# Performance work log

Hardware: AMD Instinct MI355X
Metric: run time of the kernel (lower is better)

## Reference

```python
import jax, jax.numpy as jnp
import numpy as np

LN_EPS = 1e-5
L2_EPS = 1e-6
TAU = 0.07

def _proj(x, W, b, g, be):
    # Linear + LayerNorm (dropout is identity in eval)
    y = x @ W.T + b
    mu = jnp.mean(y, axis=-1, keepdims=True)
    var = jnp.var(y, axis=-1, keepdims=True)
    return (y - mu) * jax.lax.rsqrt(var + LN_EPS) * g + be

def _l2norm(x):
    return x / (jnp.linalg.norm(x, axis=-1, keepdims=True) + L2_EPS)

def setup_inputs() -> dict:
    key = jax.random.key(0)
    ks = iter(jax.random.split(key, 16))
    B, C, D = 2048, 512, 256
    dims = {"text": 1024, "image": 1024, "audio": 512, "tab": 256}
    inp = {}
    for n, d in dims.items():
        inp[f"f_{n}"] = jax.random.normal(next(ks), (B, d), jnp.float32)
        inp[f"W_{n}"] = jax.random.normal(next(ks), (D, d), jnp.float32) * (1.0 / np.sqrt(d))
        inp[f"b_{n}"] = jnp.zeros((D,), jnp.float32)
        inp[f"g_{n}"] = jnp.ones((D,), jnp.float32)
        inp[f"be_{n}"] = jnp.zeros((D,), jnp.float32)
    inp["U"] = jax.random.normal(next(ks), (C, D), jnp.float32) * (1.0 / np.sqrt(D))
    inp["O"] = jax.random.normal(next(ks), (C, D), jnp.float32) * (1.0 / np.sqrt(D))
    inp["cls_bias"] = jnp.zeros((C,), jnp.float32)
    return inp

def reference(f_text, f_image, f_audio, f_tab,
              W_text, b_text, g_text, be_text,
              W_image, b_image, g_image, be_image,
              W_audio, b_audio, g_audio, be_audio,
              W_tab, b_tab, g_tab, be_tab,
              U, O, cls_bias):
    # Per-modality projection -> Z: [B, M, D]
    Z = jnp.stack([
        _proj(f_text, W_text, b_text, g_text, be_text),
        _proj(f_image, W_image, b_image, g_image, be_image),
        _proj(f_audio, W_audio, b_audio, g_audio, be_audio),
        _proj(f_tab, W_tab, b_tab, g_tab, be_tab),
    ], axis=1)
    Zn = _l2norm(Z)            # [B, M, D]
    Un = _l2norm(U)            # [C, D]
    sim = jnp.einsum('bmd,cd->bmc', Zn, Un) / max(TAU, 1e-6)
    r = jax.nn.softmax(sim, axis=1)                 # softmax over modalities M
    Cmix = jnp.einsum('bmc,bmd->bcd', r, Z)         # [B, C, D]
    logits = jnp.einsum('cd,bcd->bc', O, Cmix) + cls_bias
    OjZi = jnp.einsum('cd,bmd->bmc', O, Z)
    contrib = OjZi * r
    return logits, r, sim, contrib
```

## Files before the change

kernel.cpp:

```cpp
#include <hip/hip_runtime.h>
#include <math.h>

typedef __attribute__((ext_vector_type(8))) short short8;
typedef __attribute__((ext_vector_type(4))) float f32x4;
typedef unsigned short u16;

constexpr int Bn = 2048, Mn = 4, Cn = 512, Dn = 256;
constexpr size_t LOGITS_OFF = 0;
constexpr size_t R_OFF   = (size_t)Bn * Cn;
constexpr size_t SIM_OFF = R_OFF + (size_t)Bn * Mn * Cn;
constexpr size_t CTR_OFF = SIM_OFF + (size_t)Bn * Mn * Cn;
constexpr float INV_TAU = 1.0f / 0.07f;

__device__ __forceinline__ unsigned short f2bf(float f) {
  unsigned u = __float_as_uint(f);
  u += 0x7fffu + ((u >> 16) & 1u);
  return (unsigned short)(u >> 16);
}

__device__ __forceinline__ void gload16(const void* g, void* l) {
  __builtin_amdgcn_global_load_lds(
      (const __attribute__((address_space(1))) void*)g,
      (__attribute__((address_space(3))) void*)l, 16, 0, 0);
}

struct CvtArgs {
  const float* src[6];
  u16* dst[6];
};

__global__ __launch_bounds__(256) void cvt_kernel(CvtArgs a,
                                                  const float* __restrict__ U,
                                                  float* __restrict__ invU) {
  const int blk = blockIdx.x;
  if (blk >= 480) {
    int c = (blk - 480) * 4 + (threadIdx.x >> 6);
    int lane = threadIdx.x & 63;
    float4 v = *(const float4*)&U[(size_t)c * Dn + lane * 4];
    float s = v.x*v.x + v.y*v.y + v.z*v.z + v.w*v.w;
    #pragma unroll
    for (int m = 32; m >= 1; m >>= 1) s += __shfl_xor(s, m, 64);
    if (lane == 0) invU[c] = 1.0f / (sqrtf(s) + 1e-6f);
    return;
  }
  int c = blk * 256 + threadIdx.x;
  const int ends[6] = {32768, 65536, 81920, 90112, 106496, 122880};
  int ai = 0, base = 0;
  #pragma unroll
  for (int i = 0; i < 5; i++)
    if (c >= ends[i]) { ai = i + 1; base = ends[i]; }
  int idx = (c - base) * 8;
  const float4* s = (const float4*)(a.src[ai] + idx);
  float4 v0 = s[0], v1 = s[1];
  uint4 p;
  p.x = f2bf(v0.x) | ((unsigned)f2bf(v0.y) << 16);
  p.y = f2bf(v0.z) | ((unsigned)f2bf(v0.w) << 16);
  p.z = f2bf(v1.x) | ((unsigned)f2bf(v1.y) << 16);
  p.w = f2bf(v1.z) | ((unsigned)f2bf(v1.w) << 16);
  *(uint4*)(a.dst[ai] + idx) = p;
}

struct ProjArgs {
  const float* f[4];
  const float* b[4];
  const float* g[4];
  const float* be[4];
  const u16* Wb[4];
  int K[4];
};

__global__ __launch_bounds__(512, 4) void proj_kernel(ProjArgs a,
                                                      u16* __restrict__ Zb,
                                                      float* __restrict__ invZ) {
  const int m = blockIdx.y;
  const int K = a.K[m];
  const int NS = K >> 5;
  const float* __restrict__ F = a.f[m];
  const u16* __restrict__ Wm = a.Wb[m];

  const int tid = threadIdx.x;
  const int w = tid >> 6, l = tid & 63;
  const int rg = l >> 4, c16 = l & 15;
  const int row0 = blockIdx.x * 16;

  __shared__ u16 aS[16 * 1024];
  __shared__ float pS[8][16][2];
  __shared__ float qS[8][16];
  __shared__ u16 zS[16][264];

  const int niter = (K * 16) >> 12;
  for (int it = 0; it < niter; it++) {
    int i = it * 512 + tid;
    int row = i & 15, kc = i >> 4;
    const float* src = F + (size_t)(row0 + row) * K + kc * 8;
    float4 v0 = *(const float4*)src;
    float4 v1 = *(const float4*)(src + 4);
    short8 p;
    p[0] = (short)f2bf(v0.x); p[1] = (short)f2bf(v0.y);
    p[2] = (short)f2bf(v0.z); p[3] = (short)f2bf(v0.w);
    p[4] = (short)f2bf(v1.x); p[5] = (short)f2bf(v1.y);
    p[6] = (short)f2bf(v1.z); p[7] = (short)f2bf(v1.w);
    *(short8*)&aS[i * 8] = p;
  }
  __syncthreads();

  f32x4 acc[2];
  acc[0] = (f32x4){0.f, 0.f, 0.f, 0.f};
  acc[1] = (f32x4){0.f, 0.f, 0.f, 0.f};
  const u16* b0p = Wm + (size_t)(w * 32 + c16) * K + rg * 8;
  const u16* b1p = b0p + (size_t)16 * K;
  const int abase = (rg * 16 + c16) * 8;

  #pragma unroll 4
  for (int t = 0; t < NS; t++) {
    short8 av = *(const short8*)&aS[abase + t * 512];
    short8 b0 = *(const short8*)(b0p + t * 32);
    short8 b1 = *(const short8*)(b1p + t * 32);
    acc[0] = __builtin_amdgcn_mfma_f32_16x16x32_bf16(av, b0, acc[0], 0, 0, 0);
    acc[1] = __builtin_amdgcn_mfma_f32_16x16x32_bf16(av, b1, acc[1], 0, 0, 0);
  }

  float bb[2], gg[2], ee[2];
  #pragma unroll
  for (int nf = 0; nf < 2; nf++) {
    int col = w * 32 + nf * 16 + c16;
    bb[nf] = a.b[m][col];
    gg[nf] = a.g[m][col];
    ee[nf] = a.be[m][col];
  }
  float s[4] = {0,0,0,0}, s2[4] = {0,0,0,0};
  #pragma unroll
  for (int nf = 0; nf < 2; nf++)
    #pragma unroll
    for (int j = 0; j < 4; j++) {
      float y = acc[nf][j] + bb[nf];
      acc[nf][j] = y;
      s[j] += y; s2[j] += y * y;
    }
  #pragma unroll
  for (int msk = 8; msk >= 1; msk >>= 1)
    #pragma unroll
    for (int j = 0; j < 4; j++) {
      s[j]  += __shfl_xor(s[j],  msk, 64);
      s2[j] += __shfl_xor(s2[j], msk, 64);
    }
  if (c16 == 0)
    #pragma unroll
    for (int j = 0; j < 4; j++) {
      pS[w][rg*4+j][0] = s[j];
      pS[w][rg*4+j][1] = s2[j];
    }
  __syncthreads();
  float mu[4], rs[4];
  #pragma unroll
  for (int j = 0; j < 4; j++) {
    int row = rg*4 + j;
    float st = 0.f, s2t = 0.f;
    #pragma unroll
    for (int ww = 0; ww < 8; ww++) { st += pS[ww][row][0]; s2t += pS[ww][row][1]; }
    mu[j] = st * (1.0f/256.0f);
    float var = s2t * (1.0f/256.0f) - mu[j]*mu[j];
    rs[j] = rsqrtf(var + 1e-5f);
  }
  float zs[4] = {0,0,0,0};
  #pragma unroll
  for (int nf = 0; nf < 2; nf++)
    #pragma unroll
    for (int j = 0; j < 4; j++) {
      float z = (acc[nf][j] - mu[j]) * rs[j] * gg[nf] + ee[nf];
      acc[nf][j] = z;
      zs[j] += z * z;
    }
  #pragma unroll
  for (int msk = 8; msk >= 1; msk >>= 1)
    #pragma unroll
    for (int j = 0; j < 4; j++) zs[j] += __shfl_xor(zs[j], msk, 64);
  if (c16 == 0)
    #pragma unroll
    for (int j = 0; j < 4; j++) qS[w][rg*4+j] = zs[j];
  __syncthreads();
  #pragma unroll
  for (int j = 0; j < 4; j++) {
    int row = rg*4 + j;
    float zt = 0.f;
    #pragma unroll
    for (int ww = 0; ww < 8; ww++) zt += qS[ww][row];
    float inv = 1.0f / (sqrtf(zt) + 1e-6f);
    if (c16 == 0 && w == 0)
      invZ[(size_t)(row0 + row) * 4 + m] = inv;
  }
  #pragma unroll
  for (int nf = 0; nf < 2; nf++)
    #pragma unroll
    for (int j = 0; j < 4; j++)
      zS[rg*4 + j][w*32 + nf*16 + c16] = f2bf(acc[nf][j]);
  __syncthreads();
  {
    int row = tid >> 5, colc = (tid & 31) * 8;
    uint4 v = *(const uint4*)&zS[row][colc];
    *(uint4*)(Zb + ((size_t)(row0 + row) * 4 + m) * 256 + colc) = v;
  }
}

__global__ __launch_bounds__(256, 4) void dual_kernel(
    const u16* __restrict__ Zb,
    const u16* __restrict__ Ub,
    const u16* __restrict__ Ob,
    const float* __restrict__ invZ, const float* __restrict__ invU,
    const float* __restrict__ cls_bias, float* __restrict__ out) {
  const int tid = threadIdx.x;
  const int w = tid >> 6, l = tid & 63;
  const int wr = w & 1, wc = w >> 1;
  const int rg = l >> 4, c16 = l & 15;
  const int row0 = blockIdx.x * 64;
  const int col0 = blockIdx.y * 64 + wc * 32;

  __shared__ u16 aS[64 * 256];

  #pragma unroll
  for (int it = 0; it < 8; it++) {
    int i = it * 256 + tid;
    gload16(Zb + (size_t)(row0 + (i & 63)) * 256 + (i >> 6) * 8, &aS[i * 8]);
  }
  __syncthreads();

  f32x4 accU[2][2], accO[2][2];
  #pragma unroll
  for (int i = 0; i < 2; i++)
    #pragma unroll
    for (int j = 0; j < 2; j++) {
      accU[i][j] = (f32x4){0.f, 0.f, 0.f, 0.f};
      accO[i][j] = (f32x4){0.f, 0.f, 0.f, 0.f};
    }
  const u16* u0p = Ub + (size_t)(col0 + c16) * 256 + rg * 8;
  const u16* u1p = u0p + 16 * 256;
  const u16* o0p = Ob + (size_t)(col0 + c16) * 256 + rg * 8;
  const u16* o1p = o0p + 16 * 256;
  const int ab0 = (rg * 64 + wr * 32 + c16) * 8;
  const int ab1 = ab0 + 16 * 8;

  #pragma unroll 4
  for (int t = 0; t < 8; t++) {
    short8 a0 = *(const short8*)&aS[ab0 + t * 2048];
    short8 a1 = *(const short8*)&aS[ab1 + t * 2048];
    short8 u0 = *(const short8*)(u0p + t * 32);
    short8 u1 = *(const short8*)(u1p + t * 32);
    short8 o0 = *(const short8*)(o0p + t * 32);
    short8 o1 = *(const short8*)(o1p + t * 32);
    accU[0][0] = __builtin_amdgcn_mfma_f32_16x16x32_bf16(a0, u0, accU[0][0], 0, 0, 0);
    accU[0][1] = __builtin_amdgcn_mfma_f32_16x16x32_bf16(a0, u1, accU[0][1], 0, 0, 0);
    accU[1][0] = __builtin_amdgcn_mfma_f32_16x16x32_bf16(a1, u0, accU[1][0], 0, 0, 0);
    accU[1][1] = __builtin_amdgcn_mfma_f32_16x16x32_bf16(a1, u1, accU[1][1], 0, 0, 0);
    accO[0][0] = __builtin_amdgcn_mfma_f32_16x16x32_bf16(a0, o0, accO[0][0], 0, 0, 0);
    accO[0][1] = __builtin_amdgcn_mfma_f32_16x16x32_bf16(a0, o1, accO[0][1], 0, 0, 0);
    accO[1][0] = __builtin_amdgcn_mfma_f32_16x16x32_bf16(a1, o0, accO[1][0], 0, 0, 0);
    accO[1][1] = __builtin_amdgcn_mfma_f32_16x16x32_bf16(a1, o1, accO[1][1], 0, 0, 0);
  }

  #pragma unroll
  for (int mf = 0; mf < 2; mf++) {
    const int bmb = row0 + wr * 32 + mf * 16 + rg * 4;
    const f32x4 iz = *(const f32x4*)&invZ[bmb];
    const int bidx = bmb >> 2;
    #pragma unroll
    for (int nf = 0; nf < 2; nf++) {
      int col = col0 + nf * 16 + c16;
      float iu = invU[col] * INV_TAU;
      f32x4 sU = accU[mf][nf], sO = accO[mf][nf];
      float sim0 = sU[0] * iz[0] * iu;
      float sim1 = sU[1] * iz[1] * iu;
      float sim2 = sU[2] * iz[2] * iu;
      float sim3 = sU[3] * iz[3] * iu;
      float mx = fmaxf(fmaxf(sim0, sim1), fmaxf(sim2, sim3));
      float e0 = __expf(sim0 - mx), e1 = __expf(sim1 - mx);
      float e2 = __expf(sim2 - mx), e3 = __expf(sim3 - mx);
      float rinv = 1.0f / (e0 + e1 + e2 + e3);
      float r0 = e0 * rinv, r1 = e1 * rinv, r2 = e2 * rinv, r3 = e3 * rinv;
      float ct0 = sO[0] * r0, ct1 = sO[1] * r1, ct2 = sO[2] * r2, ct3 = sO[3] * r3;
      size_t sb = (size_t)bmb * Cn + col;
      out[SIM_OFF + sb]        = sim0;
      out[SIM_OFF + sb + Cn]   = sim1;
      out[SIM_OFF + sb + 2*Cn] = sim2;
      out[SIM_OFF + sb + 3*Cn] = sim3;
      out[R_OFF + sb]          = r0;
      out[R_OFF + sb + Cn]     = r1;
      out[R_OFF + sb + 2*Cn]   = r2;
      out[R_OFF + sb + 3*Cn]   = r3;
      out[CTR_OFF + sb]        = ct0;
      out[CTR_OFF + sb + Cn]   = ct1;
      out[CTR_OFF + sb + 2*Cn] = ct2;
      out[CTR_OFF + sb + 3*Cn] = ct3;
      out[LOGITS_OFF + (size_t)bidx * Cn + col] =
          ct0 + ct1 + ct2 + ct3 + cls_bias[col];
    }
  }
}

extern "C" void kernel_launch(void* const* d_in, const int* in_sizes, int n_in,
                              void* d_out, int out_size, void* d_ws, size_t ws_size,
                              hipStream_t stream) {
  const int fi[4] = {0, 5, 10, 15};
  const int Ks[4] = {1024, 1024, 512, 256};

  char* ws = (char*)d_ws;
  u16* Zb  = (u16*)(ws + 0);
  u16* Wb0 = (u16*)(ws + 4194304);
  u16* Wb1 = (u16*)(ws + 4718592);
  u16* Wb2 = (u16*)(ws + 5242880);
  u16* Wb3 = (u16*)(ws + 5505024);
  u16* Ub  = (u16*)(ws + 5636096);
  u16* Ob  = (u16*)(ws + 5898240);
  float* invZ = (float*)(ws + 6160384);
  float* invU = (float*)(ws + 6193152);
  u16* Wb[4] = {Wb0, Wb1, Wb2, Wb3};

  ProjArgs pa;
  for (int m = 0; m < 4; m++) {
    pa.f[m]  = (const float*)d_in[fi[m] + 0];
    pa.b[m]  = (const float*)d_in[fi[m] + 2];
    pa.g[m]  = (const float*)d_in[fi[m] + 3];
    pa.be[m] = (const float*)d_in[fi[m] + 4];
    pa.Wb[m] = Wb[m];
    pa.K[m]  = Ks[m];
  }
  const float* U        = (const float*)d_in[20];
  const float* O        = (const float*)d_in[21];
  const float* cls_bias = (const float*)d_in[22];

  CvtArgs ca;
  ca.src[0] = (const float*)d_in[1];   ca.dst[0] = Wb0;
  ca.src[1] = (const float*)d_in[6];   ca.dst[1] = Wb1;
  ca.src[2] = (const float*)d_in[11];  ca.dst[2] = Wb2;
  ca.src[3] = (const float*)d_in[16];  ca.dst[3] = Wb3;
  ca.src[4] = U;                       ca.dst[4] = Ub;
  ca.src[5] = O;                       ca.dst[5] = Ob;

  float* out = (float*)d_out;

  cvt_kernel<<<608, 256, 0, stream>>>(ca, U, invU);
  proj_kernel<<<dim3(Bn / 16, 4), 512, 0, stream>>>(pa, Zb, invZ);
  dual_kernel<<<dim3((Bn * Mn) / 64, Cn / 64), 256, 0, stream>>>(
      Zb, Ub, Ob, invZ, invU, cls_bias, out);
}
```

Before: 171.4 us.

## Pre-swizzle weights and Z into MFMA fragment order, retile proj and dual kernels

The convert kernel now writes the bf16 weights, U and O in MFMA-fragment order, so each lane's B operand is one contiguous 16-byte load. The projection kernel handles 32 rows per block with a 2x2 MFMA tile, which halves weight re-reads, and writes Z in a fragment-swizzled layout. The dual kernel stages U/O tiles in LDS and streams Z fragments straight from global memory, with one 16-row group per wave and a 32-column tile. The cost is larger LDS use in proj, which may lower occupancy, and more complex index math.

```diff
diff --git a/kernel.cpp b/kernel.cpp
--- a/kernel.cpp
+++ b/kernel.cpp
@@ -12,6 +12,8 @@
 constexpr size_t CTR_OFF = SIM_OFF + (size_t)Bn * Mn * Cn;
 constexpr float INV_TAU = 1.0f / 0.07f;
 
+#define MFMA16(av, bv, cv) __builtin_amdgcn_mfma_f32_16x16x32_bf16(av, bv, cv, 0, 0, 0)
+
 __device__ __forceinline__ unsigned short f2bf(float f) {
   unsigned u = __float_as_uint(f);
   u += 0x7fffu + ((u >> 16) & 1u);
@@ -23,6 +25,7 @@
       (const __attribute__((address_space(1))) void*)g,
       (__attribute__((address_space(3))) void*)l, 16, 0, 0);
 }
+
 
 struct CvtArgs {
   const float* src[6];
@@ -45,19 +48,28 @@
   }
   int c = blk * 256 + threadIdx.x;
   const int ends[6] = {32768, 65536, 81920, 90112, 106496, 122880};
+  const int Kv[6]   = {1024, 1024, 512, 256, 256, 256};
+  const int lgNT[6] = {5, 5, 4, 3, 3, 3};
   int ai = 0, base = 0;
   #pragma unroll
   for (int i = 0; i < 5; i++)
     if (c >= ends[i]) { ai = i + 1; base = ends[i]; }
-  int idx = (c - base) * 8;
-  const float4* s = (const float4*)(a.src[ai] + idx);
-  float4 v0 = s[0], v1 = s[1];
+  const int K = Kv[ai], lg = lgNT[ai];
+  int j = c - base;
+  int l = j & 63;
+  int tcg = j >> 6;
+  int t = tcg & ((1 << lg) - 1);
+  int cg = tcg >> lg;
+  int col = cg * 16 + (l & 15);
+  int k0 = t * 32 + (l >> 4) * 8;
+  const float* s = a.src[ai] + (size_t)col * K + k0;
+  float4 v0 = *(const float4*)s, v1 = *(const float4*)(s + 4);
   uint4 p;
   p.x = f2bf(v0.x) | ((unsigned)f2bf(v0.y) << 16);
   p.y = f2bf(v0.z) | ((unsigned)f2bf(v0.w) << 16);
   p.z = f2bf(v1.x) | ((unsigned)f2bf(v1.y) << 16);
   p.w = f2bf(v1.z) | ((unsigned)f2bf(v1.w) << 16);
-  *(uint4*)(a.dst[ai] + idx) = p;
+  *(uint4*)(a.dst[ai] + (size_t)j * 8) = p;
 }
 
 struct ProjArgs {
@@ -65,59 +77,61 @@
   const float* b[4];
   const float* g[4];
   const float* be[4];
-  const u16* Wb[4];
+  const u16* Wt[4];
   int K[4];
 };
 
 __global__ __launch_bounds__(512, 4) void proj_kernel(ProjArgs a,
-                                                      u16* __restrict__ Zb,
+                                                      u16* __restrict__ Zb2,
                                                       float* __restrict__ invZ) {
   const int m = blockIdx.y;
   const int K = a.K[m];
-  const int NS = K >> 5;
+  const int NT = K >> 5;
   const float* __restrict__ F = a.f[m];
-  const u16* __restrict__ Wm = a.Wb[m];
+  const u16* __restrict__ Wt = a.Wt[m];
 
   const int tid = threadIdx.x;
   const int w = tid >> 6, l = tid & 63;
   const int rg = l >> 4, c16 = l & 15;
-  const int row0 = blockIdx.x * 16;
-
-  __shared__ u16 aS[16 * 1024];
-  __shared__ float pS[8][16][2];
-  __shared__ float qS[8][16];
-  __shared__ u16 zS[16][264];
-
-  const int niter = (K * 16) >> 12;
-  for (int it = 0; it < niter; it++) {
-    int i = it * 512 + tid;
-    int row = i & 15, kc = i >> 4;
+  const int row0 = blockIdx.x * 32;
+
+  __shared__ __align__(16) u16 aS[32768];
+  __shared__ float pS[8][32][2];
+  __shared__ float qS[8][32];
+
+  const int nch = K * 4;
+  for (int i = tid; i < nch; i += 512) {
+    int row = i & 31, kc = i >> 5;
     const float* src = F + (size_t)(row0 + row) * K + kc * 8;
-    float4 v0 = *(const float4*)src;
-    float4 v1 = *(const float4*)(src + 4);
+    float4 v0 = *(const float4*)src, v1 = *(const float4*)(src + 4);
     short8 p;
     p[0] = (short)f2bf(v0.x); p[1] = (short)f2bf(v0.y);
     p[2] = (short)f2bf(v0.z); p[3] = (short)f2bf(v0.w);
     p[4] = (short)f2bf(v1.x); p[5] = (short)f2bf(v1.y);
     p[6] = (short)f2bf(v1.z); p[7] = (short)f2bf(v1.w);
-    *(short8*)&aS[i * 8] = p;
-  }
-  __syncthreads();
-
-  f32x4 acc[2];
-  acc[0] = (f32x4){0.f, 0.f, 0.f, 0.f};
-  acc[1] = (f32x4){0.f, 0.f, 0.f, 0.f};
-  const u16* b0p = Wm + (size_t)(w * 32 + c16) * K + rg * 8;
-  const u16* b1p = b0p + (size_t)16 * K;
-  const int abase = (rg * 16 + c16) * 8;
+    *(short8*)&aS[(size_t)i * 8] = p;
+  }
+  __syncthreads();
+
+  f32x4 acc[2][2];
+  #pragma unroll
+  for (int i = 0; i < 2; i++)
+    #pragma unroll
+    for (int j = 0; j < 2; j++) acc[i][j] = (f32x4){0.f, 0.f, 0.f, 0.f};
+
+  const size_t bbase = ((size_t)(w * 2) * NT) * 512 + l * 8;
+  const int a0b = rg * 256 + c16 * 8;
 
   #pragma unroll 4
-  for (int t = 0; t < NS; t++) {
-    short8 av = *(const short8*)&aS[abase + t * 512];
-    short8 b0 = *(const short8*)(b0p + t * 32);
-    short8 b1 = *(const short8*)(b1p + t * 32);
-    acc[0] = __builtin_amdgcn_mfma_f32_16x16x32_bf16(av, b0, acc[0], 0, 0, 0);
-    acc[1] = __builtin_amdgcn_mfma_f32_16x16x32_bf16(av, b1, acc[1], 0, 0, 0);
+  for (int t = 0; t < NT; t++) {
+    short8 a0 = *(const short8*)&aS[a0b + t * 1024];
+    short8 a1 = *(const short8*)&aS[a0b + t * 1024 + 128];
+    short8 b0 = *(const short8*)(Wt + bbase + (size_t)t * 512);
+    short8 b1 = *(const short8*)(Wt + bbase + (size_t)(NT + t) * 512);
+    acc[0][0] = MFMA16(a0, b0, acc[0][0]);
+    acc[0][1] = MFMA16(a0, b1, acc[0][1]);
+    acc[1][0] = MFMA16(a1, b0, acc[1][0]);
+    acc[1][1] = MFMA16(a1, b1, acc[1][1]);
   }
 
   float bb[2], gg[2], ee[2];
@@ -128,171 +142,180 @@
     gg[nf] = a.g[m][col];
     ee[nf] = a.be[m][col];
   }
-  float s[4] = {0,0,0,0}, s2[4] = {0,0,0,0};
-  #pragma unroll
-  for (int nf = 0; nf < 2; nf++)
+  float s[2][4] = {{0,0,0,0},{0,0,0,0}}, s2[2][4] = {{0,0,0,0},{0,0,0,0}};
+  #pragma unroll
+  for (int mf = 0; mf < 2; mf++)
+    #pragma unroll
+    for (int nf = 0; nf < 2; nf++)
+      #pragma unroll
+      for (int j = 0; j < 4; j++) {
+        float y = acc[mf][nf][j] + bb[nf];
+        acc[mf][nf][j] = y;
+        s[mf][j] += y; s2[mf][j] += y * y;
+      }
+  #pragma unroll
+  for (int msk = 8; msk >= 1; msk >>= 1)
+    #pragma unroll
+    for (int mf = 0; mf < 2; mf++)
+      #pragma unroll
+      for (int j = 0; j < 4; j++) {
+        s[mf][j]  += __shfl_xor(s[mf][j],  msk, 64);
+        s2[mf][j] += __shfl_xor(s2[mf][j], msk, 64);
+      }
+  if (c16 == 0)
+    #pragma unroll
+    for (int mf = 0; mf < 2; mf++)
+      #pragma unroll
+      for (int j = 0; j < 4; j++) {
+        int row = mf * 16 + rg * 4 + j;
+        pS[w][row][0] = s[mf][j];
+        pS[w][row][1] = s2[mf][j];
+      }
+  __syncthreads();
+  float mu[2][4], rs[2][4];
+  #pragma unroll
+  for (int mf = 0; mf < 2; mf++)
     #pragma unroll
     for (int j = 0; j < 4; j++) {
-      float y = acc[nf][j] + bb[nf];
-      acc[nf][j] = y;
-      s[j] += y; s2[j] += y * y;
+      int row = mf * 16 + rg * 4 + j;
+      float st = 0.f, s2t = 0.f;
+      #pragma unroll
+      for (int ww = 0; ww < 8; ww++) { st += pS[ww][row][0]; s2t += pS[ww][row][1]; }
+      mu[mf][j] = st * (1.0f / 256.0f);
+      float var = s2t * (1.0f / 256.0f) - mu[mf][j] * mu[mf][j];
+      rs[mf][j] = rsqrtf(var + 1e-5f);
     }
+  float zs[2][4] = {{0,0,0,0},{0,0,0,0}};
+  #pragma unroll
+  for (int mf = 0; mf < 2; mf++)
+    #pragma unroll
+    for (int nf = 0; nf < 2; nf++)
+      #pragma unroll
+      for (int j = 0; j < 4; j++) {
+        float z = (acc[mf][nf][j] - mu[mf][j]) * rs[mf][j] * gg[nf] + ee[nf];
+        acc[mf][nf][j] = z;
+        zs[mf][j] += z * z;
+      }
   #pragma unroll
   for (int msk = 8; msk >= 1; msk >>= 1)
     #pragma unroll
-    for (int j = 0; j < 4; j++) {
-      s[j]  += __shfl_xor(s[j],  msk, 64);
-      s2[j] += __shfl_xor(s2[j], msk, 64);
-    }
+    for (int mf = 0; mf < 2; mf++)
+      #pragma unroll
+      for (int j = 0; j < 4; j++) zs[mf][j] += __shfl_xor(zs[mf][j], msk, 64);
   if (c16 == 0)
     #pragma unroll
-    for (int j = 0; j < 4; j++) {
-      pS[w][rg*4+j][0] = s[j];
-      pS[w][rg*4+j][1] = s2[j];
-    }
-  __syncthreads();
-  float mu[4], rs[4];
-  #pragma unroll
-  for (int j = 0; j < 4; j++) {
-    int row = rg*4 + j;
-    float st = 0.f, s2t = 0.f;
-    #pragma unroll
-    for (int ww = 0; ww < 8; ww++) { st += pS[ww][row][0]; s2t += pS[ww][row][1]; }
-    mu[j] = st * (1.0f/256.0f);
-    float var = s2t * (1.0f/256.0f) - mu[j]*mu[j];
-    rs[j] = rsqrtf(var + 1e-5f);
-  }
-  float zs[4] = {0,0,0,0};
-  #pragma unroll
-  for (int nf = 0; nf < 2; nf++)
-    #pragma unroll
-    for (int j = 0; j < 4; j++) {
-      float z = (acc[nf][j] - mu[j]) * rs[j] * gg[nf] + ee[nf];
-      acc[nf][j] = z;
-      zs[j] += z * z;
-    }
-  #pragma unroll
-  for (int msk = 8; msk >= 1; msk >>= 1)
-    #pragma unroll
-    for (int j = 0; j < 4; j++) zs[j] += __shfl_xor(zs[j], msk, 64);
-  if (c16 == 0)
-    #pragma unroll
-    for (int j = 0; j < 4; j++) qS[w][rg*4+j] = zs[j];
-  __syncthreads();
-  #pragma unroll
-  for (int j = 0; j < 4; j++) {
-    int row = rg*4 + j;
-    float zt = 0.f;
-    #pragma unroll
-    for (int ww = 0; ww < 8; ww++) zt += qS[ww][row];
-    float inv = 1.0f / (sqrtf(zt) + 1e-6f);
-    if (c16 == 0 && w == 0)
-      invZ[(size_t)(row0 + row) * 4 + m] = inv;
-  }
-  #pragma unroll
-  for (int nf = 0; nf < 2; nf++)
-    #pragma unroll
-    for (int j = 0; j < 4; j++)
-      zS[rg*4 + j][w*32 + nf*16 + c16] = f2bf(acc[nf][j]);
-  __syncthreads();
-  {
-    int row = tid >> 5, colc = (tid & 31) * 8;
-    uint4 v = *(const uint4*)&zS[row][colc];
-    *(uint4*)(Zb + ((size_t)(row0 + row) * 4 + m) * 256 + colc) = v;
+    for (int mf = 0; mf < 2; mf++)
+      #pragma unroll
+      for (int j = 0; j < 4; j++) qS[w][mf * 16 + rg * 4 + j] = zs[mf][j];
+  __syncthreads();
+  if (w == 0 && c16 == 0)
+    #pragma unroll
+    for (int mf = 0; mf < 2; mf++)
+      #pragma unroll
+      for (int j = 0; j < 4; j++) {
+        int row = mf * 16 + rg * 4 + j;
+        float zt = 0.f;
+        #pragma unroll
+        for (int ww = 0; ww < 8; ww++) zt += qS[ww][row];
+        invZ[(size_t)(row0 + row) * 4 + m] = 1.0f / (sqrtf(zt) + 1e-6f);
+      }
+
+  u16 (*zS)[264] = (u16 (*)[264])aS;
+  #pragma unroll
+  for (int mf = 0; mf < 2; mf++)
+    #pragma unroll
+    for (int nf = 0; nf < 2; nf++)
+      #pragma unroll
+      for (int j = 0; j < 4; j++)
+        zS[mf * 16 + rg * 4 + j][w * 32 + nf * 16 + c16] = f2bf(acc[mf][nf][j]);
+  __syncthreads();
+  #pragma unroll
+  for (int it = 0; it < 2; it++) {
+    int cI = it * 512 + tid;
+    int i = cI & 3, rgs = (cI >> 2) & 3, t = (cI >> 4) & 7, gsub = cI >> 7;
+    int lrow = gsub * 4 + i;
+    uint4 v = *(const uint4*)&zS[lrow][t * 32 + rgs * 8];
+    size_t off = ((size_t)((blockIdx.x * 8 + gsub) * 8 + t) * 64 +
+                  rgs * 16 + i * 4 + m) * 8;
+    *(uint4*)(Zb2 + off) = v;
   }
 }
 
 __global__ __launch_bounds__(256, 4) void dual_kernel(
-    const u16* __restrict__ Zb,
-    const u16* __restrict__ Ub,
-    const u16* __restrict__ Ob,
+    const u16* __restrict__ Zb2,
+    const u16* __restrict__ Ut,
+    const u16* __restrict__ Ot,
     const float* __restrict__ invZ, const float* __restrict__ invU,
     const float* __restrict__ cls_bias, float* __restrict__ out) {
   const int tid = threadIdx.x;
   const int w = tid >> 6, l = tid & 63;
-  const int wr = w & 1, wc = w >> 1;
   const int rg = l >> 4, c16 = l & 15;
-  const int row0 = blockIdx.x * 64;
-  const int col0 = blockIdx.y * 64 + wc * 32;
-
-  __shared__ u16 aS[64 * 256];
-
-  #pragma unroll
-  for (int it = 0; it < 8; it++) {
-    int i = it * 256 + tid;
-    gload16(Zb + (size_t)(row0 + (i & 63)) * 256 + (i >> 6) * 8, &aS[i * 8]);
-  }
-  __syncthreads();
-
-  f32x4 accU[2][2], accO[2][2];
-  #pragma unroll
-  for (int i = 0; i < 2; i++)
-    #pragma unroll
-    for (int j = 0; j < 2; j++) {
-      accU[i][j] = (f32x4){0.f, 0.f, 0.f, 0.f};
-      accO[i][j] = (f32x4){0.f, 0.f, 0.f, 0.f};
-    }
-  const u16* u0p = Ub + (size_t)(col0 + c16) * 256 + rg * 8;
-  const u16* u1p = u0p + 16 * 256;
-  const u16* o0p = Ob + (size_t)(col0 + c16) * 256 + rg * 8;
-  const u16* o1p = o0p + 16 * 256;
-  const int ab0 = (rg * 64 + wr * 32 + c16) * 8;
-  const int ab1 = ab0 + 16 * 8;
+  const int g = blockIdx.x * 4 + w;
+  const int col0 = blockIdx.y * 32;
+
+  __shared__ __align__(16) u16 uS[8192];
+  __shared__ __align__(16) u16 oS[8192];
+
+  const size_t bsrc = (size_t)blockIdx.y * 8192;
+  #pragma unroll
+  for (int it = 0; it < 4; it++) {
+    int chunk = it * 256 + w * 64;
+    gload16(Ut + bsrc + (size_t)(chunk + l) * 8, &uS[(size_t)chunk * 8]);
+    gload16(Ot + bsrc + (size_t)(chunk + l) * 8, &oS[(size_t)chunk * 8]);
+  }
+  __syncthreads();
+
+  f32x4 aU[2], aO[2];
+  aU[0] = (f32x4){0.f,0.f,0.f,0.f}; aU[1] = (f32x4){0.f,0.f,0.f,0.f};
+  aO[0] = (f32x4){0.f,0.f,0.f,0.f}; aO[1] = (f32x4){0.f,0.f,0.f,0.f};
+  const u16* ap = Zb2 + ((size_t)g * 512 + l) * 8;
 
   #pragma unroll 4
   for (int t = 0; t < 8; t++) {
-    short8 a0 = *(const short8*)&aS[ab0 + t * 2048];
-    short8 a1 = *(const short8*)&aS[ab1 + t * 2048];
-    short8 u0 = *(const short8*)(u0p + t * 32);
-    short8 u1 = *(const short8*)(u1p + t * 32);
-    short8 o0 = *(const short8*)(o0p + t * 32);
-    short8 o1 = *(const short8*)(o1p + t * 32);
-    accU[0][0] = __builtin_amdgcn_mfma_f32_16x16x32_bf16(a0, u0, accU[0][0], 0, 0, 0);
-    accU[0][1] = __builtin_amdgcn_mfma_f32_16x16x32_bf16(a0, u1, accU[0][1], 0, 0, 0);
-    accU[1][0] = __builtin_amdgcn_mfma_f32_16x16x32_bf16(a1, u0, accU[1][0], 0, 0, 0);
-    accU[1][1] = __builtin_amdgcn_mfma_f32_16x16x32_bf16(a1, u1, accU[1][1], 0, 0, 0);
-    accO[0][0] = __builtin_amdgcn_mfma_f32_16x16x32_bf16(a0, o0, accO[0][0], 0, 0, 0);
-    accO[0][1] = __builtin_amdgcn_mfma_f32_16x16x32_bf16(a0, o1, accO[0][1], 0, 0, 0);
-    accO[1][0] = __builtin_amdgcn_mfma_f32_16x16x32_bf16(a1, o0, accO[1][0], 0, 0, 0);
-    accO[1][1] = __builtin_amdgcn_mfma_f32_16x16x32_bf16(a1, o1, accO[1][1], 0, 0, 0);
-  }
-
-  #pragma unroll
-  for (int mf = 0; mf < 2; mf++) {
-    const int bmb = row0 + wr * 32 + mf * 16 + rg * 4;
-    const f32x4 iz = *(const f32x4*)&invZ[bmb];
-    const int bidx = bmb >> 2;
-    #pragma unroll
-    for (int nf = 0; nf < 2; nf++) {
-      int col = col0 + nf * 16 + c16;
-      float iu = invU[col] * INV_TAU;
-      f32x4 sU = accU[mf][nf], sO = accO[mf][nf];
-      float sim0 = sU[0] * iz[0] * iu;
-      float sim1 = sU[1] * iz[1] * iu;
-      float sim2 = sU[2] * iz[2] * iu;
-      float sim3 = sU[3] * iz[3] * iu;
-      float mx = fmaxf(fmaxf(sim0, sim1), fmaxf(sim2, sim3));
-      float e0 = __expf(sim0 - mx), e1 = __expf(sim1 - mx);
-      float e2 = __expf(sim2 - mx), e3 = __expf(sim3 - mx);
-      float rinv = 1.0f / (e0 + e1 + e2 + e3);
-      float r0 = e0 * rinv, r1 = e1 * rinv, r2 = e2 * rinv, r3 = e3 * rinv;
-      float ct0 = sO[0] * r0, ct1 = sO[1] * r1, ct2 = sO[2] * r2, ct3 = sO[3] * r3;
-      size_t sb = (size_t)bmb * Cn + col;
-      out[SIM_OFF + sb]        = sim0;
-      out[SIM_OFF + sb + Cn]   = sim1;
-      out[SIM_OFF + sb + 2*Cn] = sim2;
-      out[SIM_OFF + sb + 3*Cn] = sim3;
-      out[R_OFF + sb]          = r0;
-      out[R_OFF + sb + Cn]     = r1;
-      out[R_OFF + sb + 2*Cn]   = r2;
-      out[R_OFF + sb + 3*Cn]   = r3;
-      out[CTR_OFF + sb]        = ct0;
-      out[CTR_OFF + sb + Cn]   = ct1;
-      out[CTR_OFF + sb + 2*Cn] = ct2;
-      out[CTR_OFF + sb + 3*Cn] = ct3;
-      out[LOGITS_OFF + (size_t)bidx * Cn + col] =
-          ct0 + ct1 + ct2 + ct3 + cls_bias[col];
-    }
+    short8 av = *(const short8*)(ap + (size_t)t * 512);
+    short8 u0 = *(const short8*)&uS[(size_t)t * 512 + l * 8];
+    short8 u1 = *(const short8*)&uS[(size_t)(8 + t) * 512 + l * 8];
+    short8 o0 = *(const short8*)&oS[(size_t)t * 512 + l * 8];
+    short8 o1 = *(const short8*)&oS[(size_t)(8 + t) * 512 + l * 8];
+    aU[0] = MFMA16(av, u0, aU[0]);
+    aU[1] = MFMA16(av, u1, aU[1]);
+    aO[0] = MFMA16(av, o0, aO[0]);
+    aO[1] = MFMA16(av, o1, aO[1]);
+  }
+
+  const int bmb = g * 16 + rg * 4;
+  const f32x4 iz = *(const f32x4*)&invZ[bmb];
+  const int bidx = g * 4 + rg;
+  #pragma unroll
+  for (int nf = 0; nf < 2; nf++) {
+    int col = col0 + nf * 16 + c16;
+    float iu = invU[col] * INV_TAU;
+    f32x4 sU = aU[nf], sO = aO[nf];
+    float sim0 = sU[0] * iz[0] * iu;
+    float sim1 = sU[1] * iz[1] * iu;
+    float sim2 = sU[2] * iz[2] * iu;
+    float sim3 = sU[3] * iz[3] * iu;
+    float mx = fmaxf(fmaxf(sim0, sim1), fmaxf(sim2, sim3));
+    float e0 = __expf(sim0 - mx), e1 = __expf(sim1 - mx);
+    float e2 = __expf(sim2 - mx), e3 = __expf(sim3 - mx);
+    float rinv = 1.0f / (e0 + e1 + e2 + e3);
+    float r0 = e0 * rinv, r1 = e1 * rinv, r2 = e2 * rinv, r3 = e3 * rinv;
+    float ct0 = sO[0] * r0, ct1 = sO[1] * r1, ct2 = sO[2] * r2, ct3 = sO[3] * r3;
+    size_t sb = (size_t)bmb * Cn + col;
+    out[SIM_OFF + sb]        = sim0;
+    out[SIM_OFF + sb + Cn]   = sim1;
+    out[SIM_OFF + sb + 2*Cn] = sim2;
+    out[SIM_OFF + sb + 3*Cn] = sim3;
+    out[R_OFF + sb]          = r0;
+    out[R_OFF + sb + Cn]     = r1;
+    out[R_OFF + sb + 2*Cn]   = r2;
+    out[R_OFF + sb + 3*Cn]   = r3;
+    out[CTR_OFF + sb]        = ct0;
+    out[CTR_OFF + sb + Cn]   = ct1;
+    out[CTR_OFF + sb + 2*Cn] = ct2;
+    out[CTR_OFF + sb + 3*Cn] = ct3;
+    out[LOGITS_OFF + (size_t)bidx * Cn + col] =
+        ct0 + ct1 + ct2 + ct3 + cls_bias[col];
   }
 }
 
@@ -303,16 +326,16 @@
   const int Ks[4] = {1024, 1024, 512, 256};
 
   char* ws = (char*)d_ws;
-  u16* Zb  = (u16*)(ws + 0);
-  u16* Wb0 = (u16*)(ws + 4194304);
-  u16* Wb1 = (u16*)(ws + 4718592);
-  u16* Wb2 = (u16*)(ws + 5242880);
-  u16* Wb3 = (u16*)(ws + 5505024);
-  u16* Ub  = (u16*)(ws + 5636096);
-  u16* Ob  = (u16*)(ws + 5898240);
+  u16* Zb2 = (u16*)(ws + 0);
+  u16* Wt0 = (u16*)(ws + 4194304);
+  u16* Wt1 = (u16*)(ws + 4718592);
+  u16* Wt2 = (u16*)(ws + 5242880);
+  u16* Wt3 = (u16*)(ws + 5505024);
+  u16* Ut  = (u16*)(ws + 5636096);
+  u16* Ot  = (u16*)(ws + 5898240);
   float* invZ = (float*)(ws + 6160384);
   float* invU = (float*)(ws + 6193152);
-  u16* Wb[4] = {Wb0, Wb1, Wb2, Wb3};
+  u16* Wt[4] = {Wt0, Wt1, Wt2, Wt3};
 
   ProjArgs pa;
   for (int m = 0; m < 4; m++) {
@@ -320,7 +343,7 @@
     pa.b[m]  = (const float*)d_in[fi[m] + 2];
     pa.g[m]  = (const float*)d_in[fi[m] + 3];
     pa.be[m] = (const float*)d_in[fi[m] + 4];
-    pa.Wb[m] = Wb[m];
+    pa.Wt[m] = Wt[m];
     pa.K[m]  = Ks[m];
   }
   const float* U        = (const float*)d_in[20];
@@ -328,17 +351,17 @@
   const float* cls_bias = (const float*)d_in[22];
 
   CvtArgs ca;
-  ca.src[0] = (const float*)d_in[1];   ca.dst[0] = Wb0;
-  ca.src[1] = (const float*)d_in[6];   ca.dst[1] = Wb1;
-  ca.src[2] = (const float*)d_in[11];  ca.dst[2] = Wb2;
-  ca.src[3] = (const float*)d_in[16];  ca.dst[3] = Wb3;
-  ca.src[4] = U;                       ca.dst[4] = Ub;
-  ca.src[5] = O;                       ca.dst[5] = Ob;
+  ca.src[0] = (const float*)d_in[1];   ca.dst[0] = Wt0;
+  ca.src[1] = (const float*)d_in[6];   ca.dst[1] = Wt1;
+  ca.src[2] = (const float*)d_in[11];  ca.dst[2] = Wt2;
+  ca.src[3] = (const float*)d_in[16];  ca.dst[3] = Wt3;
+  ca.src[4] = U;                       ca.dst[4] = Ut;
+  ca.src[5] = O;                       ca.dst[5] = Ot;
 
   float* out = (float*)d_out;
 
   cvt_kernel<<<608, 256, 0, stream>>>(ca, U, invU);
-  proj_kernel<<<dim3(Bn / 16, 4), 512, 0, stream>>>(pa, Zb, invZ);
-  dual_kernel<<<dim3((Bn * Mn) / 64, Cn / 64), 256, 0, stream>>>(
-      Zb, Ub, Ob, invZ, invU, cls_bias, out);
-}
+  proj_kernel<<<dim3(Bn / 32, 4), 512, 0, stream>>>(pa, Zb2, invZ);
+  dual_kernel<<<dim3((Bn * Mn) / 64, Cn / 32), 256, 0, stream>>>(
+      Zb2, Ut, Ot, invZ, invU, cls_bias, out);
+}
```

After: 159.7 us. 1.07x faster.
